# Kernel tuning notes

Measured on AMD Instinct MI355X. Metric: run time of the kernel, lower is better.

The kernel has to match this reference:

```python
import jax, jax.numpy as jnp
import numpy as np

EPS_LN1 = 1e-6   # partial(nn.LayerNorm, eps=1e-6)
EPS_OUT = 1e-5   # nn.LayerNorm default inside SS3D out_norm


def _layernorm(x, w, b, eps):
    m = jnp.mean(x, axis=-1, keepdims=True)
    v = jnp.var(x, axis=-1, keepdims=True)
    return (x - m) * jax.lax.rsqrt(v + eps) * w + b


def _selective_scan(dA, dBx):
    # dA, dBx: (B, K, d, L, N); linear recurrence h_t = dA_t * h_{t-1} + dBx_t
    def comb(c1, c2):
        a1, b1 = c1
        a2, b2 = c2
        return a2 * a1, a2 * b1 + b2
    _, hs = jax.lax.associative_scan(comb, (dA, dBx), axis=3)
    return hs  # (B, K, d, L, N)


def setup_inputs() -> dict:
    key = jax.random.key(0)
    ks = jax.random.split(key, 12)
    B, D, H, W, C = 1, 16, 16, 16, 96
    d, N, K, R = 96, 16, 6, 6  # d_inner, d_state, n_scan_dirs, dt_rank
    s = 0.02
    f = lambda k, shp: jax.random.normal(k, shp, dtype=jnp.float32)
    return {
        "x": f(ks[0], (B, D, H, W, C)),
        "ln1_w": jnp.ones((C,), jnp.float32),
        "ln1_b": jnp.zeros((C,), jnp.float32),
        "in_proj_w": f(ks[1], (2 * d, C)) * s,
        "conv_w": f(ks[2], (d, 1, 3, 3, 3)) * s,
        "conv_b": f(ks[3], (d,)) * s,
        "x_proj_w": f(ks[4], (K, R + 2 * N, d)) * s,
        "dt_proj_w": f(ks[5], (K, d, R)) * s,
        "dt_proj_b": f(ks[6], (K, d)) * s,
        "A_log": jnp.log(1.0 + 15.0 * jax.random.uniform(ks[7], (K, d, N), jnp.float32)),
        "D_skip": f(ks[8], (K, d)) * s,
        "out_norm_w": jnp.ones((d,), jnp.float32),
        "out_norm_b": jnp.zeros((d,), jnp.float32),
        "out_proj_w": f(ks[9], (C, d)) * s,
    }


def reference(x, ln1_w, ln1_b, in_proj_w, conv_w, conv_b, x_proj_w,
              dt_proj_w, dt_proj_b, A_log, D_skip, out_norm_w, out_norm_b,
              out_proj_w):
    B, D, H, W, C = x.shape
    L = D * H * W
    K, _, d = x_proj_w.shape
    R = dt_proj_w.shape[2]
    N = A_log.shape[2]

    # pre-norm
    xn = _layernorm(x, ln1_w, ln1_b, EPS_LN1)

    # in_proj -> (x, z)
    xz = jnp.einsum('bdhwc,ec->bdhwe', xn, in_proj_w)  # (B,D,H,W,2d)
    xh, z = jnp.split(xz, 2, axis=-1)

    # depthwise 3x3x3 conv + SiLU, channels-first
    xc = jnp.transpose(xh, (0, 4, 1, 2, 3))  # (B,d,D,H,W)
    xc = jax.lax.conv_general_dilated(
        xc, conv_w, window_strides=(1, 1, 1), padding='SAME',
        dimension_numbers=('NCDHW', 'OIDHW', 'NCDHW'),
        feature_group_count=d)
    xc = jax.nn.silu(xc + conv_b[None, :, None, None, None])

    # K = 6 scan orderings: DHW, HWD, WDH and their reverses
    o0 = xc.reshape(B, d, L)
    o1 = jnp.transpose(xc, (0, 1, 3, 4, 2)).reshape(B, d, L)  # (H,W,D) order
    o2 = jnp.transpose(xc, (0, 1, 4, 2, 3)).reshape(B, d, L)  # (W,D,H) order
    fwd3 = jnp.stack([o0, o1, o2], axis=1)                    # (B,3,d,L)
    xs = jnp.concatenate([fwd3, jnp.flip(fwd3, axis=-1)], axis=1)  # (B,K,d,L)

    # per-direction input-dependent parameters
    x_dbl = jnp.einsum('bkdl,kcd->bkcl', xs, x_proj_w)        # (B,K,R+2N,L)
    dt, Bm, Cm = jnp.split(x_dbl, [R, R + N], axis=2)
    dts = jnp.einsum('bkrl,kdr->bkdl', dt, dt_proj_w) + dt_proj_b[None, :, :, None]
    dts = jax.nn.softplus(dts)                                # delta_softplus

    A = -jnp.exp(A_log)                                       # (K,d,N)
    dA = jnp.exp(dts[..., None] * A[None, :, :, None, :])     # (B,K,d,L,N)
    Bt = jnp.transpose(Bm, (0, 1, 3, 2))                      # (B,K,L,N)
    dBx = (dts * xs)[..., None] * Bt[:, :, None, :, :]        # (B,K,d,L,N)

    hs = _selective_scan(dA, dBx)                             # (B,K,d,L,N)
    Ct = jnp.transpose(Cm, (0, 1, 3, 2))                      # (B,K,L,N)
    ys = jnp.einsum('bkdln,bkln->bkdl', hs, Ct) + D_skip[None, :, :, None] * xs

    # undo reversals and orderings, sum the 6 paths
    yf = ys[:, :3] + jnp.flip(ys[:, 3:], axis=-1)             # (B,3,d,L)
    y0 = yf[:, 0]
    y1 = jnp.transpose(yf[:, 1].reshape(B, d, H, W, D), (0, 1, 4, 2, 3)).reshape(B, d, L)
    y2 = jnp.transpose(yf[:, 2].reshape(B, d, W, D, H), (0, 1, 3, 4, 2)).reshape(B, d, L)
    y = (y0 + y1 + y2).reshape(B, d, D, H, W)
    y = jnp.transpose(y, (0, 2, 3, 4, 1))                     # (B,D,H,W,d)

    # out_norm, gate, out_proj
    y = _layernorm(y, out_norm_w, out_norm_b, EPS_OUT)
    y = y * jax.nn.silu(z)
    out = jnp.einsum('bdhwe,ce->bdhwc', y, out_proj_w)

    # residual (drop_path is identity at eval)
    return x + out
```

## Files before the change

### kernel.cpp

```cpp
#include <hip/hip_runtime.h>
#include <hip/hip_bf16.h>

#define L 4096
#define CDIM 96
#define DDIM 96
#define KDIR 6
#define NST 16
#define RRK 6
#define YH 32
#define NCHUNK 256
#define CHLEN 16

typedef _Float16 half4v __attribute__((ext_vector_type(4)));

__device__ __forceinline__ float sigmoidf_(float x) { return 1.f / (1.f + __expf(-x)); }

__device__ __forceinline__ int sigma_k(int kb, int l) {
    if (kb == 0) return l;
    if (kb == 1) return ((l & 15) << 8) | ((l >> 8) << 4) | ((l >> 4) & 15);
    return (((l >> 4) & 15) << 8) | ((l & 15) << 4) | (l >> 8);
}

__global__ void __launch_bounds__(192) k1_ln_inproj(
        const float* __restrict__ x, const float* __restrict__ ln_w,
        const float* __restrict__ ln_b, const float* __restrict__ Wp,
        _Float16* __restrict__ xhh, _Float16* __restrict__ zsh) {
    int s0 = blockIdx.x * 8;
    int tid = threadIdx.x;
    __shared__ __align__(16) float xt[8][96];
    __shared__ __align__(16) float xn[8][96];
    __shared__ float mss[8], rss[8];
    ((float4*)&xt[0][0])[tid] = ((const float4*)(x + (size_t)s0 * 96))[tid];
    __syncthreads();
    int wave = tid >> 6, lane = tid & 63;
    for (int r = wave; r < 8; r += 3) {
        float v = xt[r][lane] + ((lane < 32) ? xt[r][64 + lane] : 0.f);
#pragma unroll
        for (int off = 1; off < 64; off <<= 1) v += __shfl_xor(v, off);
        float vs = xt[r][lane] * xt[r][lane] + ((lane < 32) ? xt[r][64 + lane] * xt[r][64 + lane] : 0.f);
#pragma unroll
        for (int off = 1; off < 64; off <<= 1) vs += __shfl_xor(vs, off);
        if (lane == 0) {
            float mean = v * (1.f / 96.f);
            float var = vs * (1.f / 96.f) - mean * mean;
            mss[r] = mean; rss[r] = rsqrtf(var + 1e-6f);
        }
    }
    __syncthreads();
    {
        int r = tid / 24, c4 = tid % 24;
        float4 xv = ((float4*)&xt[r][0])[c4];
        float4 wv = ((const float4*)ln_w)[c4];
        float4 bv = ((const float4*)ln_b)[c4];
        float m = mss[r], rs = rss[r];
        float4 o;
        o.x = (xv.x - m) * rs * wv.x + bv.x;
        o.y = (xv.y - m) * rs * wv.y + bv.y;
        o.z = (xv.z - m) * rs * wv.z + bv.z;
        o.w = (xv.w - m) * rs * wv.w + bv.w;
        ((float4*)&xn[r][0])[c4] = o;
    }
    float4 Wr[24];
    const float4* wr = (const float4*)(Wp + (size_t)tid * 96);
#pragma unroll
    for (int c4 = 0; c4 < 24; c4++) Wr[c4] = wr[c4];
    __syncthreads();
#pragma unroll
    for (int s = 0; s < 8; s++) {
        const float4* xr4 = (const float4*)&xn[s][0];
        float a0 = 0.f, a1 = 0.f, a2 = 0.f, a3 = 0.f;
#pragma unroll
        for (int c4 = 0; c4 < 24; c4 += 4) {
            float4 x0 = xr4[c4], x1 = xr4[c4 + 1], x2 = xr4[c4 + 2], x3 = xr4[c4 + 3];
            a0 += Wr[c4].x * x0.x + Wr[c4].y * x0.y + Wr[c4].z * x0.z + Wr[c4].w * x0.w;
            a1 += Wr[c4+1].x * x1.x + Wr[c4+1].y * x1.y + Wr[c4+1].z * x1.z + Wr[c4+1].w * x1.w;
            a2 += Wr[c4+2].x * x2.x + Wr[c4+2].y * x2.y + Wr[c4+2].z * x2.z + Wr[c4+2].w * x2.w;
            a3 += Wr[c4+3].x * x3.x + Wr[c4+3].y * x3.y + Wr[c4+3].z * x3.z + Wr[c4+3].w * x3.w;
        }
        float acc = (a0 + a1) + (a2 + a3);
        if (tid < 96) xhh[(size_t)tid * L + s0 + s] = (_Float16)acc;
        else zsh[(size_t)(s0 + s) * 96 + (tid - 96)] = (_Float16)(acc * sigmoidf_(acc));
    }
}

__global__ void k2_conv(const _Float16* __restrict__ xhh, const float* __restrict__ cw,
                        const float* __restrict__ cb, _Float16* __restrict__ xch,
                        _Float16* __restrict__ xcTh) {
    int idx = blockIdx.x * 256 + threadIdx.x;
    int c = idx >> 12, s = idx & 4095;
    int dz = s >> 8, h = (s >> 4) & 15, w = s & 15;
    const _Float16* xin = xhh + (size_t)c * L;
    const float* wc = cw + c * 27;
    float acc = cb[c];
#pragma unroll
    for (int i = 0; i < 3; i++) {
        int z2 = dz + i - 1; if ((unsigned)z2 > 15u) continue;
#pragma unroll
        for (int j = 0; j < 3; j++) {
            int h2 = h + j - 1; if ((unsigned)h2 > 15u) continue;
#pragma unroll
            for (int kk = 0; kk < 3; kk++) {
                int w2 = w + kk - 1; if ((unsigned)w2 > 15u) continue;
                acc += (float)xin[z2 * 256 + h2 * 16 + w2] * wc[i * 9 + j * 3 + kk];
            }
        }
    }
    float r = acc * sigmoidf_(acc);
    _Float16 hr = (_Float16)r;
    xch[(size_t)c * L + s] = hr;
    xcTh[(size_t)s * 96 + c] = hr;
}

__global__ void k3_xproj(const _Float16* __restrict__ xch, const float* __restrict__ Wx,
                         const float* __restrict__ Wdt, const float* __restrict__ bdt,
                         _Float16* __restrict__ Y2h, _Float16* __restrict__ Zsh) {
    int k = blockIdx.x;
    int tid = threadIdx.x;
    int sbase = blockIdx.y * 256;
    int s = sbase + tid;
    int g = blockIdx.z;
    __shared__ float dts[256][6];
    float acc[14];
#pragma unroll
    for (int i = 0; i < 14; i++) acc[i] = 0.f;
    const float* wdt_rows = Wx + (size_t)k * 38 * DDIM;
    const float* wbc      = Wx + ((size_t)k * 38 + 6 + g * 8) * DDIM;
    for (int dd = 0; dd < 96; dd += 4) {
        float v[4];
#pragma unroll
        for (int j = 0; j < 4; j++) v[j] = (float)xch[(size_t)(dd + j) * L + s];
#pragma unroll
        for (int j = 0; j < 4; j++) {
#pragma unroll
            for (int r = 0; r < 6; r++) acc[r] += wdt_rows[r * DDIM + dd + j] * v[j];
#pragma unroll
            for (int i = 0; i < 8; i++) acc[6 + i] += wbc[i * DDIM + dd + j] * v[j];
        }
    }
    _Float16* yo = Y2h + ((size_t)k * L + s) * YH;
#pragma unroll
    for (int i = 0; i < 8; i++) yo[g * 8 + i] = (_Float16)acc[6 + i];
#pragma unroll
    for (int r = 0; r < 6; r++) dts[tid][r] = acc[r];
    __syncthreads();
    for (int i = 0; i < 24; i++) {
        int idx = i * 256 + tid;
        int dl = idx % 24;
        int sr = idx / 24;
        int d = g * 24 + dl;
        const float* wr = Wdt + ((size_t)k * 96 + d) * 6;
        float a = bdt[k * 96 + d];
#pragma unroll
        for (int r = 0; r < 6; r++) a += wr[r] * dts[sr][r];
        float sp = (a > 15.f) ? a : __logf(1.f + __expf(a));
        Zsh[((size_t)k * L + sbase + sr) * 96 + d] = (_Float16)sp;
    }
}


__global__ void __launch_bounds__(256) ka_scan(
        const _Float16* __restrict__ Zsh, const _Float16* __restrict__ xcTh,
        const _Float16* __restrict__ Y2h, const float* __restrict__ A_log,
        _Float16* __restrict__ Aah, _Float16* __restrict__ Abh) {
    int t = blockIdx.x * 256 + threadIdx.x;
    int nq = t & 3;
    int q = t >> 2;
    int d = q % 96;
    int rest = q / 96;
    int chunk = rest % NCHUNK;
    int k = rest / NCHUNK;
    int kb = (k < 3) ? k : (k - 3);
    bool flip = (k >= 3);
    float An[4];
    {
        float4 al = *(const float4*)(A_log + ((size_t)k * 96 + d) * 16 + nq * 4);
        An[0] = -__expf(al.x); An[1] = -__expf(al.y);
        An[2] = -__expf(al.z); An[3] = -__expf(al.w);
    }
    float a[4] = {1.f, 1.f, 1.f, 1.f};
    float b[4] = {0.f, 0.f, 0.f, 0.f};
    const _Float16* Zk = Zsh + (size_t)k * L * 96;
    const _Float16* Yk = Y2h + (size_t)k * L * YH;
    int l0 = chunk * CHLEN;
    for (int i = 0; i < CHLEN; i += 4) {
        int sI[4]; float dt[4], xv[4]; half4v Bh[4];
#pragma unroll
        for (int j = 0; j < 4; j++) {
            int l = l0 + i + j;
            int lp = flip ? (4095 - l) : l;
            sI[j] = sigma_k(kb, lp);
        }
#pragma unroll
        for (int j = 0; j < 4; j++) {
            dt[j] = (float)Zk[(size_t)sI[j] * 96 + d];
            xv[j] = (float)xcTh[(size_t)sI[j] * 96 + d];
            Bh[j] = *(const half4v*)(Yk + (size_t)sI[j] * YH + nq * 4);
        }
#pragma unroll
        for (int j = 0; j < 4; j++) {
            float dtx = dt[j] * xv[j];
            float e0 = __expf(dt[j] * An[0]);
            float e1 = __expf(dt[j] * An[1]);
            float e2 = __expf(dt[j] * An[2]);
            float e3 = __expf(dt[j] * An[3]);
            b[0] = e0 * b[0] + dtx * (float)Bh[j].x; a[0] *= e0;
            b[1] = e1 * b[1] + dtx * (float)Bh[j].y; a[1] *= e1;
            b[2] = e2 * b[2] + dtx * (float)Bh[j].z; a[2] *= e2;
            b[3] = e3 * b[3] + dtx * (float)Bh[j].w; a[3] *= e3;
        }
    }
    size_t o = (((size_t)k * NCHUNK + chunk) * 96 + d) * 16 + nq * 4;
    half4v ha, hb;
    ha.x = (_Float16)a[0]; ha.y = (_Float16)a[1]; ha.z = (_Float16)a[2]; ha.w = (_Float16)a[3];
    hb.x = (_Float16)b[0]; hb.y = (_Float16)b[1]; hb.z = (_Float16)b[2]; hb.w = (_Float16)b[3];
    *(half4v*)(Aah + o) = ha;
    *(half4v*)(Abh + o) = hb;
}

__global__ void __launch_bounds__(256) kb_combine(
        const _Float16* __restrict__ Aah, const _Float16* __restrict__ Abh,
        _Float16* __restrict__ Pbh) {
    int t = blockIdx.x * 256 + threadIdx.x;
    int n = t & 15;
    int rest = t >> 4;
    int d = rest % 96;
    int k = rest / 96;
    size_t base = ((size_t)k * NCHUNK * 96 + d) * 16 + n;
    const size_t cstride = 96 * 16;
    float rb = 0.f;
    for (int c0 = 0; c0 < NCHUNK; c0 += 16) {
        float av[16], bv[16];
#pragma unroll
        for (int j = 0; j < 16; j++) {
            av[j] = (float)Aah[base + (size_t)(c0 + j) * cstride];
            bv[j] = (float)Abh[base + (size_t)(c0 + j) * cstride];
        }
#pragma unroll
        for (int j = 0; j < 16; j++) {
            Pbh[base + (size_t)(c0 + j) * cstride] = (_Float16)rb;
            rb = av[j] * rb + bv[j];
        }
    }
}

__global__ void __launch_bounds__(256) kc_apply(
        const _Float16* __restrict__ Zsh, const _Float16* __restrict__ xcTh,
        const _Float16* __restrict__ Y2h, const float* __restrict__ A_log,
        const float* __restrict__ D_skip, const _Float16* __restrict__ Pbh,
        _Float16* __restrict__ ysh) {
    int t = blockIdx.x * 256 + threadIdx.x;
    int nq = t & 3;
    int q = t >> 2;
    int d = q % 96;
    int rest = q / 96;
    int chunk = rest % NCHUNK;
    int k = rest / NCHUNK;
    int kb = (k < 3) ? k : (k - 3);
    bool flip = (k >= 3);
    float An[4];
    {
        float4 al = *(const float4*)(A_log + ((size_t)k * 96 + d) * 16 + nq * 4);
        An[0] = -__expf(al.x); An[1] = -__expf(al.y);
        An[2] = -__expf(al.z); An[3] = -__expf(al.w);
    }
    float Dk = D_skip[k * DDIM + d];
    float h[4];
    {
        half4v hp = *(const half4v*)(Pbh + (((size_t)k * NCHUNK + chunk) * 96 + d) * 16 + nq * 4);
        h[0] = (float)hp.x; h[1] = (float)hp.y; h[2] = (float)hp.z; h[3] = (float)hp.w;
    }
    const _Float16* Zk = Zsh + (size_t)k * L * 96;
    const _Float16* Yk = Y2h + (size_t)k * L * YH;
    int l0 = chunk * CHLEN;
    for (int i = 0; i < CHLEN; i += 4) {
        int sI[4]; float dt[4], xv[4]; half4v Bh[4], Ch[4];
#pragma unroll
        for (int j = 0; j < 4; j++) {
            int l = l0 + i + j;
            int lp = flip ? (4095 - l) : l;
            sI[j] = sigma_k(kb, lp);
        }
#pragma unroll
        for (int j = 0; j < 4; j++) {
            dt[j] = (float)Zk[(size_t)sI[j] * 96 + d];
            xv[j] = (float)xcTh[(size_t)sI[j] * 96 + d];
            Bh[j] = *(const half4v*)(Yk + (size_t)sI[j] * YH + nq * 4);
            Ch[j] = *(const half4v*)(Yk + (size_t)sI[j] * YH + 16 + nq * 4);
        }
#pragma unroll
        for (int j = 0; j < 4; j++) {
            float dtx = dt[j] * xv[j];
            float e0 = __expf(dt[j] * An[0]);
            float e1 = __expf(dt[j] * An[1]);
            float e2 = __expf(dt[j] * An[2]);
            float e3 = __expf(dt[j] * An[3]);
            h[0] = e0 * h[0] + dtx * (float)Bh[j].x;
            h[1] = e1 * h[1] + dtx * (float)Bh[j].y;
            h[2] = e2 * h[2] + dtx * (float)Bh[j].z;
            h[3] = e3 * h[3] + dtx * (float)Bh[j].w;
            float p = h[0] * (float)Ch[j].x + h[1] * (float)Ch[j].y
                    + h[2] * (float)Ch[j].z + h[3] * (float)Ch[j].w;
            p += __shfl_xor(p, 1);
            p += __shfl_xor(p, 2);
            if (nq == 0) ysh[((size_t)sI[j] * KDIR + k) * 96 + d] = (_Float16)(p + Dk * xv[j]);
        }
    }
}

__global__ void __launch_bounds__(192) k6_out(
        const _Float16* __restrict__ ysh, const _Float16* __restrict__ zsh,
        const float* __restrict__ onw, const float* __restrict__ onb,
        const float* __restrict__ Wo, const float* __restrict__ x,
        float* __restrict__ out) {
    int s0 = blockIdx.x * 8;
    int tid = threadIdx.x;
    __shared__ __align__(16) float vt[8][96];
    __shared__ __align__(16) float gt[8][96];
    __shared__ float mss[8], rss[8];
#pragma unroll
    for (int j = 0; j < 4; j++) {
        int f = tid + j * 192;
        int sr = f / 96, c = f % 96;
        const _Float16* yr = ysh + ((size_t)(s0 + sr) * KDIR) * 96 + c;
        float v = 0.f;
#pragma unroll
        for (int k = 0; k < KDIR; k++) v += (float)yr[k * 96];
        vt[sr][c] = v;
    }
    __syncthreads();
    int wave = tid >> 6, lane = tid & 63;
    for (int r = wave; r < 8; r += 3) {
        float v = vt[r][lane] + ((lane < 32) ? vt[r][64 + lane] : 0.f);
#pragma unroll
        for (int off = 1; off < 64; off <<= 1) v += __shfl_xor(v, off);
        float vs = vt[r][lane] * vt[r][lane] + ((lane < 32) ? vt[r][64 + lane] * vt[r][64 + lane] : 0.f);
#pragma unroll
        for (int off = 1; off < 64; off <<= 1) vs += __shfl_xor(vs, off);
        if (lane == 0) {
            float mean = v * (1.f / 96.f);
            float var = vs * (1.f / 96.f) - mean * mean;
            mss[r] = mean; rss[r] = rsqrtf(var + 1e-5f);
        }
    }
    __syncthreads();
#pragma unroll
    for (int j = 0; j < 4; j++) {
        int f = tid + j * 192;
        int sr = f / 96, c = f % 96;
        float g = (vt[sr][c] - mss[sr]) * rss[sr] * onw[c] + onb[c];
        gt[sr][c] = g * (float)zsh[(size_t)(s0 + sr) * 96 + c];
    }
    int e = tid % 96, sg = tid / 96;
    float4 Wr[24];
    const float4* wr = (const float4*)(Wo + (size_t)e * 96);
#pragma unroll
    for (int c4 = 0; c4 < 24; c4++) Wr[c4] = wr[c4];
    __syncthreads();
#pragma unroll
    for (int j = 0; j < 4; j++) {
        int s = sg * 4 + j;
        const float4* g4 = (const float4*)&gt[s][0];
        float a0 = 0.f, a1 = 0.f, a2 = 0.f, a3 = 0.f;
#pragma unroll
        for (int c4 = 0; c4 < 24; c4 += 4) {
            float4 x0 = g4[c4], x1 = g4[c4 + 1], x2 = g4[c4 + 2], x3 = g4[c4 + 3];
            a0 += Wr[c4].x * x0.x + Wr[c4].y * x0.y + Wr[c4].z * x0.z + Wr[c4].w * x0.w;
            a1 += Wr[c4+1].x * x1.x + Wr[c4+1].y * x1.y + Wr[c4+1].z * x1.z + Wr[c4+1].w * x1.w;
            a2 += Wr[c4+2].x * x2.x + Wr[c4+2].y * x2.y + Wr[c4+2].z * x2.z + Wr[c4+2].w * x2.w;
            a3 += Wr[c4+3].x * x3.x + Wr[c4+3].y * x3.y + Wr[c4+3].z * x3.z + Wr[c4+3].w * x3.w;
        }
        float acc = (a0 + a1) + (a2 + a3) + x[(size_t)(s0 + s) * 96 + e];
        out[(size_t)(s0 + s) * 96 + e] = acc;
    }
}

extern "C" void kernel_launch(void* const* d_in, const int* in_sizes, int n_in,
                              void* d_out, int out_size, void* d_ws, size_t ws_size,
                              hipStream_t stream) {
    const float* x        = (const float*)d_in[0];
    const float* ln1_w    = (const float*)d_in[1];
    const float* ln1_b    = (const float*)d_in[2];
    const float* in_proj  = (const float*)d_in[3];
    const float* conv_w   = (const float*)d_in[4];
    const float* conv_b   = (const float*)d_in[5];
    const float* x_proj   = (const float*)d_in[6];
    const float* dt_w     = (const float*)d_in[7];
    const float* dt_b     = (const float*)d_in[8];
    const float* A_log    = (const float*)d_in[9];
    const float* D_skip   = (const float*)d_in[10];
    const float* onw      = (const float*)d_in[11];
    const float* onb      = (const float*)d_in[12];
    const float* out_w    = (const float*)d_in[13];
    float* out = (float*)d_out;

    _Float16* xhh  = (_Float16*)d_ws;
    _Float16* zsh  = xhh + (size_t)96 * L;
    _Float16* xch  = zsh + (size_t)96 * L;
    _Float16* xcTh = xch + (size_t)96 * L;
    _Float16* Y2h  = xcTh + (size_t)96 * L;
    _Float16* Zsh  = Y2h + (size_t)KDIR * L * YH;
    _Float16* ysh  = Zsh + (size_t)KDIR * L * 96;
    _Float16* Aah  = ysh + (size_t)L * KDIR * 96;
    _Float16* Abh  = Aah + (size_t)KDIR * NCHUNK * DDIM * NST;
    _Float16* Pbh  = Abh + (size_t)KDIR * NCHUNK * DDIM * NST;

    k1_ln_inproj<<<dim3(L / 8), dim3(192), 0, stream>>>(x, ln1_w, ln1_b, in_proj, xhh, zsh);
    k2_conv<<<dim3(96 * L / 256), dim3(256), 0, stream>>>(xhh, conv_w, conv_b, xch, xcTh);
    k3_xproj<<<dim3(KDIR, 16, 4), dim3(256), 0, stream>>>(xch, x_proj, dt_w, dt_b, Y2h, Zsh);
    ka_scan<<<dim3(KDIR * NCHUNK * DDIM * 4 / 256), dim3(256), 0, stream>>>(Zsh, xcTh, Y2h, A_log, Aah, Abh);
    kb_combine<<<dim3(KDIR * DDIM * NST / 256), dim3(256), 0, stream>>>(Aah, Abh, Pbh);
    kc_apply<<<dim3(KDIR * NCHUNK * DDIM * 4 / 256), dim3(256), 0, stream>>>(Zsh, xcTh, Y2h, A_log, D_skip, Pbh, ysh);
    k6_out<<<dim3(L / 8), dim3(192), 0, stream>>>(ysh, zsh, onw, onb, out_w, x, out);
}
```

Baseline: 178.7 us.

## Store scan inputs in per-direction scan order and precompute dt*x

k3_xproj now writes B/C, dt and a new dt*x buffer in per-direction scan order, indexed by l instead of the permuted spatial index. The two scan kernels can then read them contiguously with no sigma permutation per step. The D_skip term moves out of kc_apply into k6_out, and exp is replaced by exp2 with a prescaled A. The scan-order scatter moves into k3's writes, which are now strided, and an extra fp16 buffer adds memory traffic and a 48KB shared array in k3.

```diff
diff --git a/kernel.cpp b/kernel.cpp
--- a/kernel.cpp
+++ b/kernel.cpp
@@ -19,6 +19,15 @@
     if (kb == 0) return l;
     if (kb == 1) return ((l & 15) << 8) | ((l >> 8) << 4) | ((l >> 4) & 15);
     return (((l >> 4) & 15) << 8) | ((l & 15) << 4) | (l >> 8);
+}
+
+__device__ __forceinline__ int lrow_k(int k, int s) {
+    int kb = (k < 3) ? k : (k - 3);
+    int l;
+    if (kb == 0) l = s;
+    else if (kb == 1) l = sigma_k(2, s);
+    else l = sigma_k(1, s);
+    return (k >= 3) ? (4095 - l) : l;
 }
 
 __global__ void __launch_bounds__(192) k1_ln_inproj(
@@ -113,13 +122,15 @@
 
 __global__ void k3_xproj(const _Float16* __restrict__ xch, const float* __restrict__ Wx,
                          const float* __restrict__ Wdt, const float* __restrict__ bdt,
-                         _Float16* __restrict__ Y2h, _Float16* __restrict__ Zsh) {
+                         _Float16* __restrict__ Yl, _Float16* __restrict__ Zl,
+                         _Float16* __restrict__ dtxl) {
     int k = blockIdx.x;
     int tid = threadIdx.x;
     int sbase = blockIdx.y * 256;
     int s = sbase + tid;
     int g = blockIdx.z;
     __shared__ float dts[256][6];
+    __shared__ _Float16 xcs[96][258];
     float acc[14];
 #pragma unroll
     for (int i = 0; i < 14; i++) acc[i] = 0.f;
@@ -128,7 +139,11 @@
     for (int dd = 0; dd < 96; dd += 4) {
         float v[4];
 #pragma unroll
-        for (int j = 0; j < 4; j++) v[j] = (float)xch[(size_t)(dd + j) * L + s];
+        for (int j = 0; j < 4; j++) {
+            _Float16 hv = xch[(size_t)(dd + j) * L + s];
+            v[j] = (float)hv;
+            xcs[dd + j][tid] = hv;
+        }
 #pragma unroll
         for (int j = 0; j < 4; j++) {
 #pragma unroll
@@ -137,9 +152,12 @@
             for (int i = 0; i < 8; i++) acc[6 + i] += wbc[i * DDIM + dd + j] * v[j];
         }
     }
-    _Float16* yo = Y2h + ((size_t)k * L + s) * YH;
-#pragma unroll
-    for (int i = 0; i < 8; i++) yo[g * 8 + i] = (_Float16)acc[6 + i];
+    {
+        int lr = lrow_k(k, s);
+        _Float16* yo = Yl + ((size_t)k * L + lr) * YH;
+#pragma unroll
+        for (int i = 0; i < 8; i++) yo[g * 8 + i] = (_Float16)acc[6 + i];
+    }
 #pragma unroll
     for (int r = 0; r < 6; r++) dts[tid][r] = acc[r];
     __syncthreads();
@@ -153,14 +171,16 @@
 #pragma unroll
         for (int r = 0; r < 6; r++) a += wr[r] * dts[sr][r];
         float sp = (a > 15.f) ? a : __logf(1.f + __expf(a));
-        Zsh[((size_t)k * L + sbase + sr) * 96 + d] = (_Float16)sp;
-    }
-}
-
+        int lr = lrow_k(k, sbase + sr);
+        size_t o = ((size_t)k * L + lr) * 96 + d;
+        Zl[o] = (_Float16)sp;
+        dtxl[o] = (_Float16)(sp * (float)xcs[d][sr]);
+    }
+}
 
 __global__ void __launch_bounds__(256) ka_scan(
-        const _Float16* __restrict__ Zsh, const _Float16* __restrict__ xcTh,
-        const _Float16* __restrict__ Y2h, const float* __restrict__ A_log,
+        const _Float16* __restrict__ Zl, const _Float16* __restrict__ dtxl,
+        const _Float16* __restrict__ Yl, const float* __restrict__ A_log,
         _Float16* __restrict__ Aah, _Float16* __restrict__ Abh) {
     int t = blockIdx.x * 256 + threadIdx.x;
     int nq = t & 3;
@@ -169,44 +189,37 @@
     int rest = q / 96;
     int chunk = rest % NCHUNK;
     int k = rest / NCHUNK;
-    int kb = (k < 3) ? k : (k - 3);
-    bool flip = (k >= 3);
     float An[4];
     {
         float4 al = *(const float4*)(A_log + ((size_t)k * 96 + d) * 16 + nq * 4);
-        An[0] = -__expf(al.x); An[1] = -__expf(al.y);
-        An[2] = -__expf(al.z); An[3] = -__expf(al.w);
+        An[0] = -__expf(al.x) * 1.44269504f; An[1] = -__expf(al.y) * 1.44269504f;
+        An[2] = -__expf(al.z) * 1.44269504f; An[3] = -__expf(al.w) * 1.44269504f;
     }
     float a[4] = {1.f, 1.f, 1.f, 1.f};
     float b[4] = {0.f, 0.f, 0.f, 0.f};
-    const _Float16* Zk = Zsh + (size_t)k * L * 96;
-    const _Float16* Yk = Y2h + (size_t)k * L * YH;
+    const _Float16* Zk = Zl + (size_t)k * L * 96;
+    const _Float16* Xk = dtxl + (size_t)k * L * 96;
+    const _Float16* Yk = Yl + (size_t)k * L * YH;
     int l0 = chunk * CHLEN;
     for (int i = 0; i < CHLEN; i += 4) {
-        int sI[4]; float dt[4], xv[4]; half4v Bh[4];
+        float dt[4], dx[4]; half4v Bh[4];
 #pragma unroll
         for (int j = 0; j < 4; j++) {
             int l = l0 + i + j;
-            int lp = flip ? (4095 - l) : l;
-            sI[j] = sigma_k(kb, lp);
-        }
-#pragma unroll
-        for (int j = 0; j < 4; j++) {
-            dt[j] = (float)Zk[(size_t)sI[j] * 96 + d];
-            xv[j] = (float)xcTh[(size_t)sI[j] * 96 + d];
-            Bh[j] = *(const half4v*)(Yk + (size_t)sI[j] * YH + nq * 4);
-        }
-#pragma unroll
-        for (int j = 0; j < 4; j++) {
-            float dtx = dt[j] * xv[j];
-            float e0 = __expf(dt[j] * An[0]);
-            float e1 = __expf(dt[j] * An[1]);
-            float e2 = __expf(dt[j] * An[2]);
-            float e3 = __expf(dt[j] * An[3]);
-            b[0] = e0 * b[0] + dtx * (float)Bh[j].x; a[0] *= e0;
-            b[1] = e1 * b[1] + dtx * (float)Bh[j].y; a[1] *= e1;
-            b[2] = e2 * b[2] + dtx * (float)Bh[j].z; a[2] *= e2;
-            b[3] = e3 * b[3] + dtx * (float)Bh[j].w; a[3] *= e3;
+            dt[j] = (float)Zk[(size_t)l * 96 + d];
+            dx[j] = (float)Xk[(size_t)l * 96 + d];
+            Bh[j] = *(const half4v*)(Yk + (size_t)l * YH + nq * 4);
+        }
+#pragma unroll
+        for (int j = 0; j < 4; j++) {
+            float e0 = exp2f(dt[j] * An[0]);
+            float e1 = exp2f(dt[j] * An[1]);
+            float e2 = exp2f(dt[j] * An[2]);
+            float e3 = exp2f(dt[j] * An[3]);
+            b[0] = e0 * b[0] + dx[j] * (float)Bh[j].x; a[0] *= e0;
+            b[1] = e1 * b[1] + dx[j] * (float)Bh[j].y; a[1] *= e1;
+            b[2] = e2 * b[2] + dx[j] * (float)Bh[j].z; a[2] *= e2;
+            b[3] = e3 * b[3] + dx[j] * (float)Bh[j].w; a[3] *= e3;
         }
     }
     size_t o = (((size_t)k * NCHUNK + chunk) * 96 + d) * 16 + nq * 4;
@@ -244,10 +257,9 @@
 }
 
 __global__ void __launch_bounds__(256) kc_apply(
-        const _Float16* __restrict__ Zsh, const _Float16* __restrict__ xcTh,
-        const _Float16* __restrict__ Y2h, const float* __restrict__ A_log,
-        const float* __restrict__ D_skip, const _Float16* __restrict__ Pbh,
-        _Float16* __restrict__ ysh) {
+        const _Float16* __restrict__ Zl, const _Float16* __restrict__ dtxl,
+        const _Float16* __restrict__ Yl, const float* __restrict__ A_log,
+        const _Float16* __restrict__ Pbh, _Float16* __restrict__ ysh) {
     int t = blockIdx.x * 256 + threadIdx.x;
     int nq = t & 3;
     int q = t >> 2;
@@ -260,55 +272,55 @@
     float An[4];
     {
         float4 al = *(const float4*)(A_log + ((size_t)k * 96 + d) * 16 + nq * 4);
-        An[0] = -__expf(al.x); An[1] = -__expf(al.y);
-        An[2] = -__expf(al.z); An[3] = -__expf(al.w);
-    }
-    float Dk = D_skip[k * DDIM + d];
+        An[0] = -__expf(al.x) * 1.44269504f; An[1] = -__expf(al.y) * 1.44269504f;
+        An[2] = -__expf(al.z) * 1.44269504f; An[3] = -__expf(al.w) * 1.44269504f;
+    }
     float h[4];
     {
         half4v hp = *(const half4v*)(Pbh + (((size_t)k * NCHUNK + chunk) * 96 + d) * 16 + nq * 4);
         h[0] = (float)hp.x; h[1] = (float)hp.y; h[2] = (float)hp.z; h[3] = (float)hp.w;
     }
-    const _Float16* Zk = Zsh + (size_t)k * L * 96;
-    const _Float16* Yk = Y2h + (size_t)k * L * YH;
+    const _Float16* Zk = Zl + (size_t)k * L * 96;
+    const _Float16* Xk = dtxl + (size_t)k * L * 96;
+    const _Float16* Yk = Yl + (size_t)k * L * YH;
     int l0 = chunk * CHLEN;
     for (int i = 0; i < CHLEN; i += 4) {
-        int sI[4]; float dt[4], xv[4]; half4v Bh[4], Ch[4];
+        float dt[4], dx[4]; half4v Bh[4], Ch[4];
 #pragma unroll
         for (int j = 0; j < 4; j++) {
             int l = l0 + i + j;
-            int lp = flip ? (4095 - l) : l;
-            sI[j] = sigma_k(kb, lp);
-        }
-#pragma unroll
-        for (int j = 0; j < 4; j++) {
-            dt[j] = (float)Zk[(size_t)sI[j] * 96 + d];
-            xv[j] = (float)xcTh[(size_t)sI[j] * 96 + d];
-            Bh[j] = *(const half4v*)(Yk + (size_t)sI[j] * YH + nq * 4);
-            Ch[j] = *(const half4v*)(Yk + (size_t)sI[j] * YH + 16 + nq * 4);
-        }
-#pragma unroll
-        for (int j = 0; j < 4; j++) {
-            float dtx = dt[j] * xv[j];
-            float e0 = __expf(dt[j] * An[0]);
-            float e1 = __expf(dt[j] * An[1]);
-            float e2 = __expf(dt[j] * An[2]);
-            float e3 = __expf(dt[j] * An[3]);
-            h[0] = e0 * h[0] + dtx * (float)Bh[j].x;
-            h[1] = e1 * h[1] + dtx * (float)Bh[j].y;
-            h[2] = e2 * h[2] + dtx * (float)Bh[j].z;
-            h[3] = e3 * h[3] + dtx * (float)Bh[j].w;
+            dt[j] = (float)Zk[(size_t)l * 96 + d];
+            dx[j] = (float)Xk[(size_t)l * 96 + d];
+            Bh[j] = *(const half4v*)(Yk + (size_t)l * YH + nq * 4);
+            Ch[j] = *(const half4v*)(Yk + (size_t)l * YH + 16 + nq * 4);
+        }
+#pragma unroll
+        for (int j = 0; j < 4; j++) {
+            int l = l0 + i + j;
+            float e0 = exp2f(dt[j] * An[0]);
+            float e1 = exp2f(dt[j] * An[1]);
+            float e2 = exp2f(dt[j] * An[2]);
+            float e3 = exp2f(dt[j] * An[3]);
+            h[0] = e0 * h[0] + dx[j] * (float)Bh[j].x;
+            h[1] = e1 * h[1] + dx[j] * (float)Bh[j].y;
+            h[2] = e2 * h[2] + dx[j] * (float)Bh[j].z;
+            h[3] = e3 * h[3] + dx[j] * (float)Bh[j].w;
             float p = h[0] * (float)Ch[j].x + h[1] * (float)Ch[j].y
                     + h[2] * (float)Ch[j].z + h[3] * (float)Ch[j].w;
             p += __shfl_xor(p, 1);
             p += __shfl_xor(p, 2);
-            if (nq == 0) ysh[((size_t)sI[j] * KDIR + k) * 96 + d] = (_Float16)(p + Dk * xv[j]);
+            if (nq == 0) {
+                int lp = flip ? (4095 - l) : l;
+                int sI = sigma_k(kb, lp);
+                ysh[((size_t)sI * KDIR + k) * 96 + d] = (_Float16)p;
+            }
         }
     }
 }
 
 __global__ void __launch_bounds__(192) k6_out(
         const _Float16* __restrict__ ysh, const _Float16* __restrict__ zsh,
+        const _Float16* __restrict__ xcTh, const float* __restrict__ D_skip,
         const float* __restrict__ onw, const float* __restrict__ onb,
         const float* __restrict__ Wo, const float* __restrict__ x,
         float* __restrict__ out) {
@@ -325,6 +337,10 @@
         float v = 0.f;
 #pragma unroll
         for (int k = 0; k < KDIR; k++) v += (float)yr[k * 96];
+        float ds = 0.f;
+#pragma unroll
+        for (int k = 0; k < KDIR; k++) ds += D_skip[k * DDIM + c];
+        v += ds * (float)xcTh[(size_t)(s0 + sr) * 96 + c];
         vt[sr][c] = v;
     }
     __syncthreads();
@@ -397,18 +413,19 @@
     _Float16* zsh  = xhh + (size_t)96 * L;
     _Float16* xch  = zsh + (size_t)96 * L;
     _Float16* xcTh = xch + (size_t)96 * L;
-    _Float16* Y2h  = xcTh + (size_t)96 * L;
-    _Float16* Zsh  = Y2h + (size_t)KDIR * L * YH;
-    _Float16* ysh  = Zsh + (size_t)KDIR * L * 96;
+    _Float16* Yl   = xcTh + (size_t)96 * L;
+    _Float16* Zl   = Yl + (size_t)KDIR * L * YH;
+    _Float16* dtxl = Zl + (size_t)KDIR * L * 96;
+    _Float16* ysh  = dtxl + (size_t)KDIR * L * 96;
     _Float16* Aah  = ysh + (size_t)L * KDIR * 96;
     _Float16* Abh  = Aah + (size_t)KDIR * NCHUNK * DDIM * NST;
     _Float16* Pbh  = Abh + (size_t)KDIR * NCHUNK * DDIM * NST;
 
     k1_ln_inproj<<<dim3(L / 8), dim3(192), 0, stream>>>(x, ln1_w, ln1_b, in_proj, xhh, zsh);
     k2_conv<<<dim3(96 * L / 256), dim3(256), 0, stream>>>(xhh, conv_w, conv_b, xch, xcTh);
-    k3_xproj<<<dim3(KDIR, 16, 4), dim3(256), 0, stream>>>(xch, x_proj, dt_w, dt_b, Y2h, Zsh);
-    ka_scan<<<dim3(KDIR * NCHUNK * DDIM * 4 / 256), dim3(256), 0, stream>>>(Zsh, xcTh, Y2h, A_log, Aah, Abh);
+    k3_xproj<<<dim3(KDIR, 16, 4), dim3(256), 0, stream>>>(xch, x_proj, dt_w, dt_b, Yl, Zl, dtxl);
+    ka_scan<<<dim3(KDIR * NCHUNK * DDIM * 4 / 256), dim3(256), 0, stream>>>(Zl, dtxl, Yl, A_log, Aah, Abh);
     kb_combine<<<dim3(KDIR * DDIM * NST / 256), dim3(256), 0, stream>>>(Aah, Abh, Pbh);
-    kc_apply<<<dim3(KDIR * NCHUNK * DDIM * 4 / 256), dim3(256), 0, stream>>>(Zsh, xcTh, Y2h, A_log, D_skip, Pbh, ysh);
-    k6_out<<<dim3(L / 8), dim3(192), 0, stream>>>(ysh, zsh, onw, onb, out_w, x, out);
-}
+    kc_apply<<<dim3(KDIR * NCHUNK * DDIM * 4 / 256), dim3(256), 0, stream>>>(Zl, dtxl, Yl, A_log, Pbh, ysh);
+    k6_out<<<dim3(L / 8), dim3(192), 0, stream>>>(ysh, zsh, xcTh, D_skip, onw, onb, out_w, x, out);
+}
```

Result: slower. 184.7 us (+3.4%).
